# Kernel tuning notes

Measured on AMD Instinct MI355X. Metric: run time of the kernel, lower is better.

Reference implementation:

```python
import jax, jax.numpy as jnp
import numpy as np

# ---- static config matching init_kwargs / input_specs ----
B, H, W_IN, IN_CAPS, ATOMS = 2, 48, 48, 8, 16
KER, STRIDE, OUT_CAPS, ROUTINGS = 3, 1, 16, 3


def setup_inputs() -> dict:
    key = jax.random.key(0)
    k1, k2 = jax.random.split(key)
    x = jax.random.normal(k1, (B, H, W_IN, IN_CAPS * (ATOMS + 1)), dtype=jnp.float32)
    # W: [input_num_capsule, num_capsule, 4, 4], he_normal-ish scale (fan_in=16)
    W = jax.random.normal(k2, (IN_CAPS, OUT_CAPS, 4, 4), dtype=jnp.float32) * np.float32((2.0 / 16.0) ** 0.5)
    return {"input_tensor": x, "W": W}


def _kernel_tile(x, k=KER, stride=STRIDE):
    # Equivalent to the depthwise-conv patch-extraction trick + transpose:
    # output [B, Ho, Wo, k*k, C]
    b, h, w, c = x.shape
    ho = (h - k) // stride + 1
    wo = (w - k) // stride + 1
    patches = jnp.stack(
        [x[:, i:i + stride * ho:stride, j:j + stride * wo:stride, :]
         for i in range(k) for j in range(k)],
        axis=3,
    )
    return patches


def _squash(s, eps=1e-7):
    sq = jnp.sum(s * s, axis=-1, keepdims=True)
    return (sq / (1.0 + sq)) * s / jnp.sqrt(sq + eps)


def reference(input_tensor, W):
    t = _kernel_tile(input_tensor)                      # [B,Ho,Wo,kk,C]
    b, ho, wo, kk, c = t.shape
    n = b * ho * wo
    t = t.reshape(n, kk * IN_CAPS, ATOMS + 1)           # [N, kk*in_caps, 17]
    pose = t[..., :ATOMS].reshape(n, kk, IN_CAPS, 4, 4)
    act = t[..., ATOMS].reshape(n, kk * IN_CAPS)        # input capsule activations
    # vote transform: pose @ W per (input capsule -> output capsule)
    votes = jnp.einsum('nkiab,iobc->nkioac', pose, W)
    votes = votes.reshape(n, kk * IN_CAPS, OUT_CAPS, ATOMS)  # [N, kkin, out, 16]
    # iterative routing-by-agreement, weighted by input activation
    logits = jnp.zeros((n, kk * IN_CAPS, OUT_CAPS), dtype=votes.dtype)
    v = None
    for r in range(ROUTINGS):
        coup = jax.nn.softmax(logits, axis=2) * act[:, :, None]
        s = jnp.einsum('nko,nkoe->noe', coup, votes)    # weighted vote sum
        v = _squash(s)                                  # [N, out, 16]
        if r < ROUTINGS - 1:
            logits = logits + jnp.einsum('nkoe,noe->nko', votes, v)
    return v.reshape(b, ho, wo, OUT_CAPS, ATOMS)
```

## Files before the change

kernel.cpp:

```cpp
#include <hip/hip_runtime.h>


#define IN_CAPS 8
#define OUT_CAPS 16
#define KK 9
#define KKIN 72
#define BATCH 2
#define H_IN 48
#define W_IN 48
#define HO 46
#define WO 46
#define CIN 136
#define NPIX (BATCH*HO*WO)

typedef float v2f __attribute__((ext_vector_type(2)));
typedef float v4f __attribute__((ext_vector_type(4)));

__device__ __forceinline__ v2f lo2(v4f v) { return __builtin_shufflevector(v, v, 0, 1); }
__device__ __forceinline__ v2f hi2(v4f v) { return __builtin_shufflevector(v, v, 2, 3); }
__device__ __forceinline__ v2f fma2(v2f a, v2f b, v2f c) {
    return __builtin_elementwise_fma(a, b, c);
}

template<int CTRL>
__device__ __forceinline__ float dpp_f(float x) {
    return __int_as_float(
        __builtin_amdgcn_update_dpp(0, __float_as_int(x), CTRL, 0xF, 0xF, true));
}
__device__ __forceinline__ float row_sum16(float x) {
    x += dpp_f<0xB1>(x);
    x += dpp_f<0x4E>(x);
    x += dpp_f<0x124>(x);
    x += dpp_f<0x128>(x);
    return x;
}

__device__ __forceinline__ int pose_row(int k) {
    return k * 20 + ((k >> 3) & 1) * 4;
}
__device__ __forceinline__ int g_row(int o, int ic) {
    return (o * 8 + ic) * 20 + o * 4;
}

__global__ __launch_bounds__(256, 4)
void capsule_routing_kernel(const float* __restrict__ x,
                            const float* __restrict__ Wg,
                            float* __restrict__ out)
{
    __shared__ alignas(16) float pose_s[1440];
    __shared__ alignas(16) float pose_t[16 * 76];
    __shared__ float act_s[KKIN];
    __shared__ alignas(16) float g_s[2620];
    __shared__ alignas(16) float coup_s[OUT_CAPS * 76];

    const int tid = threadIdx.x;
    const int o = tid >> 4;
    const int e = tid & 15;
    const int c = e & 3;

    const int n   = blockIdx.x;
    const int b   = n / (HO * WO);
    const int rem = n - b * (HO * WO);
    const int ho  = rem / WO;
    const int wo  = rem - ho * WO;

    v2f w01[IN_CAPS], w23[IN_CAPS];
    #pragma unroll
    for (int i = 0; i < IN_CAPS; ++i) {
        const v4f wv = *reinterpret_cast<const v4f*>(
            &Wg[((i * OUT_CAPS + o) * 4 + c) * 4]);
        w01[i] = lo2(wv);
        w23[i] = hi2(wv);
    }

    for (int idx = tid; idx < KK * CIN; idx += 256) {
        int p  = idx / CIN;
        int cc = idx - p * CIN;
        int py = p / 3, px = p - py * 3;
        float val = x[(((b * H_IN + ho + py) * W_IN) + (wo + px)) * CIN + cc];
        int ic = cc / 17;
        int aa = cc - ic * 17;
        int k  = p * IN_CAPS + ic;
        if (aa == 16) {
            act_s[k] = val;
        } else {
            pose_s[pose_row(k) + aa] = val;
            pose_t[aa * 76 + k] = val;
        }
    }
    __syncthreads();

    if (tid < KKIN) {
        float cv = act_s[tid] * 0.0625f;
        #pragma unroll
        for (int j = 0; j < OUT_CAPS; ++j) coup_s[j * 76 + tid] = cv;
    }
    __syncthreads();

    const int kf  = tid >> 1;
    const int hf  = tid & 1;
    const int ick = kf & 7;
    float lreg8[8] = {0.f,0.f,0.f,0.f,0.f,0.f,0.f,0.f};

    const v4f* cp = reinterpret_cast<const v4f*>(&coup_s[o * 76]);
    const v4f* pp = reinterpret_cast<const v4f*>(&pose_t[e * 76]);

    float v = 0.f;
    #pragma unroll 1
    for (int r = 0; r < 3; ++r) {
        v2f M01 = {0.f,0.f}, M23 = {0.f,0.f}, M45 = {0.f,0.f}, M67 = {0.f,0.f};
        #pragma unroll
        for (int p = 0; p < KK; ++p) {
            const v4f c0 = cp[2*p], c1 = cp[2*p+1];
            const v4f q0 = pp[2*p], q1 = pp[2*p+1];
            M01 = fma2(lo2(c0), lo2(q0), M01);
            M23 = fma2(hi2(c0), hi2(q0), M23);
            M45 = fma2(lo2(c1), lo2(q1), M45);
            M67 = fma2(hi2(c1), hi2(q1), M67);
        }
        const float Mc[8] = {M01.x, M01.y, M23.x, M23.y,
                             M45.x, M45.y, M67.x, M67.y};
        v2f U01 = {0.f,0.f}, U23 = {0.f,0.f};
        #pragma unroll
        for (int ic = 0; ic < 8; ++ic) {
            const v2f mm = {Mc[ic], Mc[ic]};
            U01 = fma2(w01[ic], mm, U01);
            U23 = fma2(w23[ic], mm, U23);
        }
        float Z0 = U01.x, Z1 = U01.y, Z2 = U23.x, Z3 = U23.y;
        Z0 += dpp_f<0xB1>(Z0); Z1 += dpp_f<0xB1>(Z1);
        Z2 += dpp_f<0xB1>(Z2); Z3 += dpp_f<0xB1>(Z3);
        Z0 += dpp_f<0x4E>(Z0); Z1 += dpp_f<0x4E>(Z1);
        Z2 += dpp_f<0x4E>(Z2); Z3 += dpp_f<0x4E>(Z3);
        const float s = (c == 0) ? Z0 : (c == 1) ? Z1 : (c == 2) ? Z2 : Z3;

        const float sq = row_sum16(s * s);
        v = s * (sq / ((1.f + sq) * sqrtf(sq + 1e-7f)));

        if (r < 2) {
            const float vq0 = dpp_f<0x00>(v);
            const float vq1 = dpp_f<0x55>(v);
            const float vq2 = dpp_f<0xAA>(v);
            const float vq3 = dpp_f<0xFF>(v);
            const v2f vq01 = {vq0, vq1};
            const v2f vq23 = {vq2, vq3};
            #pragma unroll
            for (int ic = 0; ic < 8; ++ic) {
                v2f h = fma2(w23[ic], vq23, w01[ic] * vq01);
                g_s[g_row(o, ic) + e] = h.x + h.y;
            }
            __syncthreads();
            if (tid < 2 * KKIN) {
                const v4f* pk = reinterpret_cast<const v4f*>(
                    &pose_s[pose_row(kf)]);
                const v4f p0 = pk[0], p1 = pk[1], p2 = pk[2], p3 = pk[3];
                const v2f q0 = lo2(p0), q1 = hi2(p0), q2 = lo2(p1), q3 = hi2(p1);
                const v2f q4 = lo2(p2), q5 = hi2(p2), q6 = lo2(p3), q7 = hi2(p3);
                float lg[8];
                #pragma unroll
                for (int j = 0; j < 8; ++j) {
                    const int oo = hf * 8 + j;
                    const v4f* gp = reinterpret_cast<const v4f*>(
                        &g_s[g_row(oo, ick)]);
                    const v4f g0 = gp[0], g1 = gp[1], g2 = gp[2], g3 = gp[3];
                    v2f A = fma2(q2, lo2(g1), fma2(q4, lo2(g2),
                              fma2(q6, lo2(g3), q0 * lo2(g0))));
                    v2f Bv = fma2(q3, hi2(g1), fma2(q5, hi2(g2),
                              fma2(q7, hi2(g3), q1 * hi2(g0))));
                    lreg8[j] += (A.x + A.y) + (Bv.x + Bv.y);
                    lg[j] = lreg8[j];
                }
                float mx = -1e30f;
                #pragma unroll
                for (int j = 0; j < 8; ++j) mx = fmaxf(mx, lg[j]);
                mx = fmaxf(mx, dpp_f<0xB1>(mx));
                float sum = 0.f;
                #pragma unroll
                for (int j = 0; j < 8; ++j) { lg[j] = __expf(lg[j] - mx); sum += lg[j]; }
                sum += dpp_f<0xB1>(sum);
                const float scale = act_s[kf] / sum;
                #pragma unroll
                for (int j = 0; j < 8; ++j)
                    coup_s[(hf * 8 + j) * 76 + kf] = lg[j] * scale;
            }
            __syncthreads();
        }
    }

    out[n * 256 + tid] = v;
}

extern "C" void kernel_launch(void* const* d_in, const int* in_sizes, int n_in,
                              void* d_out, int out_size, void* d_ws, size_t ws_size,
                              hipStream_t stream) {
    const float* x  = (const float*)d_in[0];
    const float* Wt = (const float*)d_in[1];
    float* outp = (float*)d_out;
    capsule_routing_kernel<<<dim3(NPIX), dim3(256), 0, stream>>>(x, Wt, outp);
}
```

Before: 92.61 us.

## Peel first routing iteration to skip uniform coupling init and remap blocks

The first routing pass now reads the input activations directly and applies the uniform 1/16 softmax factor as a scalar. This removes the coup_s initialization loop and one block-wide barrier. The three routing iterations are fully unrolled, with helper lambdas for the shared parts, which grows code size. Block indices are also remapped so consecutive blocks take pixels from eight separate regions, which changes the cache-access pattern for overlapping input patches.

```diff
diff --git a/kernel.cpp b/kernel.cpp
--- a/kernel.cpp
+++ b/kernel.cpp
@@ -49,7 +49,7 @@
 {
     __shared__ alignas(16) float pose_s[1440];
     __shared__ alignas(16) float pose_t[16 * 76];
-    __shared__ float act_s[KKIN];
+    __shared__ alignas(16) float act_s[KKIN];
     __shared__ alignas(16) float g_s[2620];
     __shared__ alignas(16) float coup_s[OUT_CAPS * 76];
 
@@ -58,7 +58,9 @@
     const int e = tid & 15;
     const int c = e & 3;
 
-    const int n   = blockIdx.x;
+    const int bx = blockIdx.x;
+    const int n  = (bx & 7) * (NPIX / 8) + (bx >> 3);
+
     const int b   = n / (HO * WO);
     const int rem = n - b * (HO * WO);
     const int ho  = rem / WO;
@@ -90,13 +92,6 @@
     }
     __syncthreads();
 
-    if (tid < KKIN) {
-        float cv = act_s[tid] * 0.0625f;
-        #pragma unroll
-        for (int j = 0; j < OUT_CAPS; ++j) coup_s[j * 76 + tid] = cv;
-    }
-    __syncthreads();
-
     const int kf  = tid >> 1;
     const int hf  = tid & 1;
     const int ick = kf & 7;
@@ -104,10 +99,97 @@
 
     const v4f* cp = reinterpret_cast<const v4f*>(&coup_s[o * 76]);
     const v4f* pp = reinterpret_cast<const v4f*>(&pose_t[e * 76]);
+    const v4f* ap = reinterpret_cast<const v4f*>(act_s);
 
     float v = 0.f;
-    #pragma unroll 1
-    for (int r = 0; r < 3; ++r) {
+
+    auto finishBU = [&](v2f M01, v2f M23, v2f M45, v2f M67, float mscale) {
+        const float Mc[8] = {M01.x, M01.y, M23.x, M23.y,
+                             M45.x, M45.y, M67.x, M67.y};
+        v2f U01 = {0.f,0.f}, U23 = {0.f,0.f};
+        #pragma unroll
+        for (int ic = 0; ic < 8; ++ic) {
+            const v2f mm = {Mc[ic], Mc[ic]};
+            U01 = fma2(w01[ic], mm, U01);
+            U23 = fma2(w23[ic], mm, U23);
+        }
+        const v2f sc = {mscale, mscale};
+        U01 *= sc; U23 *= sc;
+        float Z0 = U01.x, Z1 = U01.y, Z2 = U23.x, Z3 = U23.y;
+        Z0 += dpp_f<0xB1>(Z0); Z1 += dpp_f<0xB1>(Z1);
+        Z2 += dpp_f<0xB1>(Z2); Z3 += dpp_f<0xB1>(Z3);
+        Z0 += dpp_f<0x4E>(Z0); Z1 += dpp_f<0x4E>(Z1);
+        Z2 += dpp_f<0x4E>(Z2); Z3 += dpp_f<0x4E>(Z3);
+        const float s = (c == 0) ? Z0 : (c == 1) ? Z1 : (c == 2) ? Z2 : Z3;
+        const float sq = row_sum16(s * s);
+        v = s * (sq / ((1.f + sq) * sqrtf(sq + 1e-7f)));
+    };
+
+    auto g_fused = [&]() {
+        const float vq0 = dpp_f<0x00>(v);
+        const float vq1 = dpp_f<0x55>(v);
+        const float vq2 = dpp_f<0xAA>(v);
+        const float vq3 = dpp_f<0xFF>(v);
+        const v2f vq01 = {vq0, vq1};
+        const v2f vq23 = {vq2, vq3};
+        #pragma unroll
+        for (int ic = 0; ic < 8; ++ic) {
+            v2f h = fma2(w23[ic], vq23, w01[ic] * vq01);
+            g_s[g_row(o, ic) + e] = h.x + h.y;
+        }
+        __syncthreads();
+        if (tid < 2 * KKIN) {
+            const v4f* pk = reinterpret_cast<const v4f*>(
+                &pose_s[pose_row(kf)]);
+            const v4f p0 = pk[0], p1 = pk[1], p2 = pk[2], p3 = pk[3];
+            const v2f q0 = lo2(p0), q1 = hi2(p0), q2 = lo2(p1), q3 = hi2(p1);
+            const v2f q4 = lo2(p2), q5 = hi2(p2), q6 = lo2(p3), q7 = hi2(p3);
+            float lg[8];
+            #pragma unroll
+            for (int j = 0; j < 8; ++j) {
+                const int oo = hf * 8 + j;
+                const v4f* gp = reinterpret_cast<const v4f*>(
+                    &g_s[g_row(oo, ick)]);
+                const v4f g0 = gp[0], g1 = gp[1], g2 = gp[2], g3 = gp[3];
+                v2f A = fma2(q2, lo2(g1), fma2(q4, lo2(g2),
+                          fma2(q6, lo2(g3), q0 * lo2(g0))));
+                v2f Bv = fma2(q3, hi2(g1), fma2(q5, hi2(g2),
+                          fma2(q7, hi2(g3), q1 * hi2(g0))));
+                lreg8[j] += (A.x + A.y) + (Bv.x + Bv.y);
+                lg[j] = lreg8[j];
+            }
+            float mx = -1e30f;
+            #pragma unroll
+            for (int j = 0; j < 8; ++j) mx = fmaxf(mx, lg[j]);
+            mx = fmaxf(mx, dpp_f<0xB1>(mx));
+            float sum = 0.f;
+            #pragma unroll
+            for (int j = 0; j < 8; ++j) { lg[j] = __expf(lg[j] - mx); sum += lg[j]; }
+            sum += dpp_f<0xB1>(sum);
+            const float scale = act_s[kf] / sum;
+            #pragma unroll
+            for (int j = 0; j < 8; ++j)
+                coup_s[(hf * 8 + j) * 76 + kf] = lg[j] * scale;
+        }
+        __syncthreads();
+    };
+
+    {
+        v2f M01 = {0.f,0.f}, M23 = {0.f,0.f}, M45 = {0.f,0.f}, M67 = {0.f,0.f};
+        #pragma unroll
+        for (int p = 0; p < KK; ++p) {
+            const v4f a0 = ap[2*p], a1 = ap[2*p+1];
+            const v4f q0 = pp[2*p], q1 = pp[2*p+1];
+            M01 = fma2(lo2(a0), lo2(q0), M01);
+            M23 = fma2(hi2(a0), hi2(q0), M23);
+            M45 = fma2(lo2(a1), lo2(q1), M45);
+            M67 = fma2(hi2(a1), hi2(q1), M67);
+        }
+        finishBU(M01, M23, M45, M67, 0.0625f);
+        g_fused();
+    }
+
+    {
         v2f M01 = {0.f,0.f}, M23 = {0.f,0.f}, M45 = {0.f,0.f}, M67 = {0.f,0.f};
         #pragma unroll
         for (int p = 0; p < KK; ++p) {
@@ -118,73 +200,22 @@
             M45 = fma2(lo2(c1), lo2(q1), M45);
             M67 = fma2(hi2(c1), hi2(q1), M67);
         }
-        const float Mc[8] = {M01.x, M01.y, M23.x, M23.y,
-                             M45.x, M45.y, M67.x, M67.y};
-        v2f U01 = {0.f,0.f}, U23 = {0.f,0.f};
-        #pragma unroll
-        for (int ic = 0; ic < 8; ++ic) {
-            const v2f mm = {Mc[ic], Mc[ic]};
-            U01 = fma2(w01[ic], mm, U01);
-            U23 = fma2(w23[ic], mm, U23);
-        }
-        float Z0 = U01.x, Z1 = U01.y, Z2 = U23.x, Z3 = U23.y;
-        Z0 += dpp_f<0xB1>(Z0); Z1 += dpp_f<0xB1>(Z1);
-        Z2 += dpp_f<0xB1>(Z2); Z3 += dpp_f<0xB1>(Z3);
-        Z0 += dpp_f<0x4E>(Z0); Z1 += dpp_f<0x4E>(Z1);
-        Z2 += dpp_f<0x4E>(Z2); Z3 += dpp_f<0x4E>(Z3);
-        const float s = (c == 0) ? Z0 : (c == 1) ? Z1 : (c == 2) ? Z2 : Z3;
-
-        const float sq = row_sum16(s * s);
-        v = s * (sq / ((1.f + sq) * sqrtf(sq + 1e-7f)));
-
-        if (r < 2) {
-            const float vq0 = dpp_f<0x00>(v);
-            const float vq1 = dpp_f<0x55>(v);
-            const float vq2 = dpp_f<0xAA>(v);
-            const float vq3 = dpp_f<0xFF>(v);
-            const v2f vq01 = {vq0, vq1};
-            const v2f vq23 = {vq2, vq3};
-            #pragma unroll
-            for (int ic = 0; ic < 8; ++ic) {
-                v2f h = fma2(w23[ic], vq23, w01[ic] * vq01);
-                g_s[g_row(o, ic) + e] = h.x + h.y;
-            }
-            __syncthreads();
-            if (tid < 2 * KKIN) {
-                const v4f* pk = reinterpret_cast<const v4f*>(
-                    &pose_s[pose_row(kf)]);
-                const v4f p0 = pk[0], p1 = pk[1], p2 = pk[2], p3 = pk[3];
-                const v2f q0 = lo2(p0), q1 = hi2(p0), q2 = lo2(p1), q3 = hi2(p1);
-                const v2f q4 = lo2(p2), q5 = hi2(p2), q6 = lo2(p3), q7 = hi2(p3);
-                float lg[8];
-                #pragma unroll
-                for (int j = 0; j < 8; ++j) {
-                    const int oo = hf * 8 + j;
-                    const v4f* gp = reinterpret_cast<const v4f*>(
-                        &g_s[g_row(oo, ick)]);
-                    const v4f g0 = gp[0], g1 = gp[1], g2 = gp[2], g3 = gp[3];
-                    v2f A = fma2(q2, lo2(g1), fma2(q4, lo2(g2),
-                              fma2(q6, lo2(g3), q0 * lo2(g0))));
-                    v2f Bv = fma2(q3, hi2(g1), fma2(q5, hi2(g2),
-                              fma2(q7, hi2(g3), q1 * hi2(g0))));
-                    lreg8[j] += (A.x + A.y) + (Bv.x + Bv.y);
-                    lg[j] = lreg8[j];
-                }
-                float mx = -1e30f;
-                #pragma unroll
-                for (int j = 0; j < 8; ++j) mx = fmaxf(mx, lg[j]);
-                mx = fmaxf(mx, dpp_f<0xB1>(mx));
-                float sum = 0.f;
-                #pragma unroll
-                for (int j = 0; j < 8; ++j) { lg[j] = __expf(lg[j] - mx); sum += lg[j]; }
-                sum += dpp_f<0xB1>(sum);
-                const float scale = act_s[kf] / sum;
-                #pragma unroll
-                for (int j = 0; j < 8; ++j)
-                    coup_s[(hf * 8 + j) * 76 + kf] = lg[j] * scale;
-            }
-            __syncthreads();
-        }
+        finishBU(M01, M23, M45, M67, 1.0f);
+        g_fused();
+    }
+
+    {
+        v2f M01 = {0.f,0.f}, M23 = {0.f,0.f}, M45 = {0.f,0.f}, M67 = {0.f,0.f};
+        #pragma unroll
+        for (int p = 0; p < KK; ++p) {
+            const v4f c0 = cp[2*p], c1 = cp[2*p+1];
+            const v4f q0 = pp[2*p], q1 = pp[2*p+1];
+            M01 = fma2(lo2(c0), lo2(q0), M01);
+            M23 = fma2(hi2(c0), hi2(q0), M23);
+            M45 = fma2(lo2(c1), lo2(q1), M45);
+            M67 = fma2(hi2(c1), hi2(q1), M67);
+        }
+        finishBU(M01, M23, M45, M67, 1.0f);
     }
 
     out[n * 256 + tid] = v;
```

Result: faster. 89.89 us (-2.9%).

## Process two pixels per block with XCD-aware mapping and split fused threads

Applied to the files above, without the earlier changes.

Each block now handles two adjacent output pixels, halving the grid and sharing the W register loads, while the logit/softmax stage runs both pixels at once using threads 0-143 for one and 112-255 for the other, so the two ranges overlap on threads 112-143. Block indices are remapped so each XCD gets a contiguous range of pixel pairs, which should improve L2 reuse of overlapping input patches. The first routing iteration reads the activations directly with a 1/16 scale instead of filling the coupling buffer, removing a sync. The squash norm is computed from four partial squares and two DPP steps. Shared memory doubles and occupancy drops to 3 blocks per CU, trading parallelism for more work per block.

```diff
diff --git a/kernel.cpp b/kernel.cpp
--- a/kernel.cpp
+++ b/kernel.cpp
@@ -12,6 +12,7 @@
 #define WO 46
 #define CIN 136
 #define NPIX (BATCH*HO*WO)
+#define NPAIR (NPIX/2)
 
 typedef float v2f __attribute__((ext_vector_type(2)));
 typedef float v4f __attribute__((ext_vector_type(4)));
@@ -27,13 +28,6 @@
     return __int_as_float(
         __builtin_amdgcn_update_dpp(0, __float_as_int(x), CTRL, 0xF, 0xF, true));
 }
-__device__ __forceinline__ float row_sum16(float x) {
-    x += dpp_f<0xB1>(x);
-    x += dpp_f<0x4E>(x);
-    x += dpp_f<0x124>(x);
-    x += dpp_f<0x128>(x);
-    return x;
-}
 
 __device__ __forceinline__ int pose_row(int k) {
     return k * 20 + ((k >> 3) & 1) * 4;
@@ -42,27 +36,28 @@
     return (o * 8 + ic) * 20 + o * 4;
 }
 
-__global__ __launch_bounds__(256, 4)
+__global__ __launch_bounds__(256, 3)
 void capsule_routing_kernel(const float* __restrict__ x,
                             const float* __restrict__ Wg,
                             float* __restrict__ out)
 {
-    __shared__ alignas(16) float pose_s[1440];
-    __shared__ alignas(16) float pose_t[16 * 76];
-    __shared__ float act_s[KKIN];
-    __shared__ alignas(16) float g_s[2620];
-    __shared__ alignas(16) float coup_s[OUT_CAPS * 76];
+    __shared__ alignas(16) float pose_s[2][1440];
+    __shared__ alignas(16) float pose_t[2][16 * 76];
+    __shared__ alignas(16) float act_s[2][KKIN];
+    __shared__ alignas(16) float g_s[2][2620];
+    __shared__ alignas(16) float coup_s[2][OUT_CAPS * 76];
 
     const int tid = threadIdx.x;
     const int o = tid >> 4;
     const int e = tid & 15;
     const int c = e & 3;
 
-    const int n   = blockIdx.x;
-    const int b   = n / (HO * WO);
-    const int rem = n - b * (HO * WO);
-    const int ho  = rem / WO;
-    const int wo  = rem - ho * WO;
+    const int bx  = blockIdx.x;
+    const int xcd = bx & 7;
+    const int sub = bx >> 3;
+    const int pair = (xcd < 4 ? xcd * 265 : 1060 + (xcd - 4) * 264) + sub;
+    const int n0 = pair * 2;
+    const int n1 = n0 + 1;
 
     v2f w01[IN_CAPS], w23[IN_CAPS];
     #pragma unroll
@@ -73,46 +68,47 @@
         w23[i] = hi2(wv);
     }
 
-    for (int idx = tid; idx < KK * CIN; idx += 256) {
-        int p  = idx / CIN;
-        int cc = idx - p * CIN;
-        int py = p / 3, px = p - py * 3;
-        float val = x[(((b * H_IN + ho + py) * W_IN) + (wo + px)) * CIN + cc];
-        int ic = cc / 17;
-        int aa = cc - ic * 17;
-        int k  = p * IN_CAPS + ic;
-        if (aa == 16) {
-            act_s[k] = val;
-        } else {
-            pose_s[pose_row(k) + aa] = val;
-            pose_t[aa * 76 + k] = val;
+    #pragma unroll
+    for (int p01 = 0; p01 < 2; ++p01) {
+        const int nn  = p01 ? n1 : n0;
+        const int b   = nn / (HO * WO);
+        const int rem = nn - b * (HO * WO);
+        const int ho  = rem / WO;
+        const int wo  = rem - ho * WO;
+        for (int idx = tid; idx < KK * CIN; idx += 256) {
+            int p  = idx / CIN;
+            int cc = idx - p * CIN;
+            int py = p / 3, px = p - py * 3;
+            float val = x[(((b * H_IN + ho + py) * W_IN) + (wo + px)) * CIN + cc];
+            int ic = cc / 17;
+            int aa = cc - ic * 17;
+            int k  = p * IN_CAPS + ic;
+            if (aa == 16) {
+                act_s[p01][k] = val;
+            } else {
+                pose_s[p01][pose_row(k) + aa] = val;
+                pose_t[p01][aa * 76 + k] = val;
+            }
         }
     }
     __syncthreads();
 
-    if (tid < KKIN) {
-        float cv = act_s[tid] * 0.0625f;
-        #pragma unroll
-        for (int j = 0; j < OUT_CAPS; ++j) coup_s[j * 76 + tid] = cv;
-    }
-    __syncthreads();
-
-    const int kf  = tid >> 1;
-    const int hf  = tid & 1;
-    const int ick = kf & 7;
-    float lreg8[8] = {0.f,0.f,0.f,0.f,0.f,0.f,0.f,0.f};
-
-    const v4f* cp = reinterpret_cast<const v4f*>(&coup_s[o * 76]);
-    const v4f* pp = reinterpret_cast<const v4f*>(&pose_t[e * 76]);
-
-    float v = 0.f;
-    #pragma unroll 1
-    for (int r = 0; r < 3; ++r) {
+    float lr0[8] = {0.f,0.f,0.f,0.f,0.f,0.f,0.f,0.f};
+    float lr1[8] = {0.f,0.f,0.f,0.f,0.f,0.f,0.f,0.f};
+
+    const v4f* cp0 = reinterpret_cast<const v4f*>(&coup_s[0][o * 76]);
+    const v4f* cp1 = reinterpret_cast<const v4f*>(&coup_s[1][o * 76]);
+    const v4f* pp0 = reinterpret_cast<const v4f*>(&pose_t[0][e * 76]);
+    const v4f* pp1 = reinterpret_cast<const v4f*>(&pose_t[1][e * 76]);
+    const v4f* ap0 = reinterpret_cast<const v4f*>(act_s[0]);
+    const v4f* ap1 = reinterpret_cast<const v4f*>(act_s[1]);
+
+    auto phaseB = [&](const v4f* ca, const v4f* qa, float mscale) -> float {
         v2f M01 = {0.f,0.f}, M23 = {0.f,0.f}, M45 = {0.f,0.f}, M67 = {0.f,0.f};
         #pragma unroll
         for (int p = 0; p < KK; ++p) {
-            const v4f c0 = cp[2*p], c1 = cp[2*p+1];
-            const v4f q0 = pp[2*p], q1 = pp[2*p+1];
+            const v4f c0 = ca[2*p], c1 = ca[2*p+1];
+            const v4f q0 = qa[2*p], q1 = qa[2*p+1];
             M01 = fma2(lo2(c0), lo2(q0), M01);
             M23 = fma2(hi2(c0), hi2(q0), M23);
             M45 = fma2(lo2(c1), lo2(q1), M45);
@@ -127,67 +123,92 @@
             U01 = fma2(w01[ic], mm, U01);
             U23 = fma2(w23[ic], mm, U23);
         }
+        const v2f sc = {mscale, mscale};
+        U01 *= sc; U23 *= sc;
         float Z0 = U01.x, Z1 = U01.y, Z2 = U23.x, Z3 = U23.y;
         Z0 += dpp_f<0xB1>(Z0); Z1 += dpp_f<0xB1>(Z1);
         Z2 += dpp_f<0xB1>(Z2); Z3 += dpp_f<0xB1>(Z3);
         Z0 += dpp_f<0x4E>(Z0); Z1 += dpp_f<0x4E>(Z1);
         Z2 += dpp_f<0x4E>(Z2); Z3 += dpp_f<0x4E>(Z3);
+        float t = Z0*Z0 + Z1*Z1 + Z2*Z2 + Z3*Z3;
+        t += dpp_f<0x124>(t);
+        t += dpp_f<0x128>(t);
         const float s = (c == 0) ? Z0 : (c == 1) ? Z1 : (c == 2) ? Z2 : Z3;
-
-        const float sq = row_sum16(s * s);
-        v = s * (sq / ((1.f + sq) * sqrtf(sq + 1e-7f)));
-
-        if (r < 2) {
-            const float vq0 = dpp_f<0x00>(v);
-            const float vq1 = dpp_f<0x55>(v);
-            const float vq2 = dpp_f<0xAA>(v);
-            const float vq3 = dpp_f<0xFF>(v);
-            const v2f vq01 = {vq0, vq1};
-            const v2f vq23 = {vq2, vq3};
-            #pragma unroll
-            for (int ic = 0; ic < 8; ++ic) {
-                v2f h = fma2(w23[ic], vq23, w01[ic] * vq01);
-                g_s[g_row(o, ic) + e] = h.x + h.y;
-            }
-            __syncthreads();
-            if (tid < 2 * KKIN) {
-                const v4f* pk = reinterpret_cast<const v4f*>(
-                    &pose_s[pose_row(kf)]);
-                const v4f p0 = pk[0], p1 = pk[1], p2 = pk[2], p3 = pk[3];
-                const v2f q0 = lo2(p0), q1 = hi2(p0), q2 = lo2(p1), q3 = hi2(p1);
-                const v2f q4 = lo2(p2), q5 = hi2(p2), q6 = lo2(p3), q7 = hi2(p3);
-                float lg[8];
-                #pragma unroll
-                for (int j = 0; j < 8; ++j) {
-                    const int oo = hf * 8 + j;
-                    const v4f* gp = reinterpret_cast<const v4f*>(
-                        &g_s[g_row(oo, ick)]);
-                    const v4f g0 = gp[0], g1 = gp[1], g2 = gp[2], g3 = gp[3];
-                    v2f A = fma2(q2, lo2(g1), fma2(q4, lo2(g2),
-                              fma2(q6, lo2(g3), q0 * lo2(g0))));
-                    v2f Bv = fma2(q3, hi2(g1), fma2(q5, hi2(g2),
-                              fma2(q7, hi2(g3), q1 * hi2(g0))));
-                    lreg8[j] += (A.x + A.y) + (Bv.x + Bv.y);
-                    lg[j] = lreg8[j];
-                }
-                float mx = -1e30f;
-                #pragma unroll
-                for (int j = 0; j < 8; ++j) mx = fmaxf(mx, lg[j]);
-                mx = fmaxf(mx, dpp_f<0xB1>(mx));
-                float sum = 0.f;
-                #pragma unroll
-                for (int j = 0; j < 8; ++j) { lg[j] = __expf(lg[j] - mx); sum += lg[j]; }
-                sum += dpp_f<0xB1>(sum);
-                const float scale = act_s[kf] / sum;
-                #pragma unroll
-                for (int j = 0; j < 8; ++j)
-                    coup_s[(hf * 8 + j) * 76 + kf] = lg[j] * scale;
-            }
-            __syncthreads();
-        }
-    }
-
-    out[n * 256 + tid] = v;
+        return s * (t / ((1.f + t) * sqrtf(t + 1e-7f)));
+    };
+
+    auto build_G = [&](int px, float v) {
+        const float vq0 = dpp_f<0x00>(v);
+        const float vq1 = dpp_f<0x55>(v);
+        const float vq2 = dpp_f<0xAA>(v);
+        const float vq3 = dpp_f<0xFF>(v);
+        const v2f vq01 = {vq0, vq1};
+        const v2f vq23 = {vq2, vq3};
+        #pragma unroll
+        for (int ic = 0; ic < 8; ++ic) {
+            v2f h = fma2(w23[ic], vq23, w01[ic] * vq01);
+            g_s[px][g_row(o, ic) + e] = h.x + h.y;
+        }
+    };
+
+    auto fused = [&](int px, int kf, int hf, float (&lreg)[8]) {
+        const int ick = kf & 7;
+        const v4f* pk = reinterpret_cast<const v4f*>(&pose_s[px][pose_row(kf)]);
+        const v4f p0 = pk[0], p1 = pk[1], p2 = pk[2], p3 = pk[3];
+        const v2f q0 = lo2(p0), q1 = hi2(p0), q2 = lo2(p1), q3 = hi2(p1);
+        const v2f q4 = lo2(p2), q5 = hi2(p2), q6 = lo2(p3), q7 = hi2(p3);
+        float lg[8];
+        #pragma unroll
+        for (int j = 0; j < 8; ++j) {
+            const int oo = hf * 8 + j;
+            const v4f* gp = reinterpret_cast<const v4f*>(&g_s[px][g_row(oo, ick)]);
+            const v4f g0 = gp[0], g1 = gp[1], g2 = gp[2], g3 = gp[3];
+            v2f A = fma2(q2, lo2(g1), fma2(q4, lo2(g2),
+                      fma2(q6, lo2(g3), q0 * lo2(g0))));
+            v2f Bv = fma2(q3, hi2(g1), fma2(q5, hi2(g2),
+                      fma2(q7, hi2(g3), q1 * hi2(g0))));
+            lreg[j] += (A.x + A.y) + (Bv.x + Bv.y);
+            lg[j] = lreg[j];
+        }
+        float mx = -1e30f;
+        #pragma unroll
+        for (int j = 0; j < 8; ++j) mx = fmaxf(mx, lg[j]);
+        mx = fmaxf(mx, dpp_f<0xB1>(mx));
+        float sum = 0.f;
+        #pragma unroll
+        for (int j = 0; j < 8; ++j) { lg[j] = __expf(lg[j] - mx); sum += lg[j]; }
+        sum += dpp_f<0xB1>(sum);
+        const float scale = act_s[px][kf] / sum;
+        #pragma unroll
+        for (int j = 0; j < 8; ++j)
+            coup_s[px][(hf * 8 + j) * 76 + kf] = lg[j] * scale;
+    };
+
+    float v0, v1;
+
+    v0 = phaseB(ap0, pp0, 0.0625f);
+    v1 = phaseB(ap1, pp1, 0.0625f);
+    build_G(0, v0);
+    build_G(1, v1);
+    __syncthreads();
+    if (tid < 2 * KKIN)  fused(0, tid >> 1, tid & 1, lr0);
+    if (tid >= 112) { const int t1 = tid - 112; fused(1, t1 >> 1, t1 & 1, lr1); }
+    __syncthreads();
+
+    v0 = phaseB(cp0, pp0, 1.0f);
+    v1 = phaseB(cp1, pp1, 1.0f);
+    build_G(0, v0);
+    build_G(1, v1);
+    __syncthreads();
+    if (tid < 2 * KKIN)  fused(0, tid >> 1, tid & 1, lr0);
+    if (tid >= 112) { const int t1 = tid - 112; fused(1, t1 >> 1, t1 & 1, lr1); }
+    __syncthreads();
+
+    v0 = phaseB(cp0, pp0, 1.0f);
+    v1 = phaseB(cp1, pp1, 1.0f);
+
+    out[n0 * 256 + tid] = v0;
+    out[n1 * 256 + tid] = v1;
 }
 
 extern "C" void kernel_launch(void* const* d_in, const int* in_sizes, int n_in,
@@ -196,5 +217,5 @@
     const float* x  = (const float*)d_in[0];
     const float* Wt = (const float*)d_in[1];
     float* outp = (float*)d_out;
-    capsule_routing_kernel<<<dim3(NPIX), dim3(256), 0, stream>>>(x, Wt, outp);
-}
+    capsule_routing_kernel<<<dim3(NPAIR), dim3(256), 0, stream>>>(x, Wt, outp);
+}
```

New measurement: 95.94 us. +3.6%, slower.
